# Performance work log

Measured on AMD Instinct MI355X. Metric: run time of the kernel, lower is better.

## Reference

```python
import jax, jax.numpy as jnp
import numpy as np
from jax import lax

W_BITS = (8, 8, 8)  # per init_kwargs
BN_EPS = 1e-5
DN = ('NCHW', 'OIHW', 'NCHW')


def fake_quant(w, bits):
    # Symmetric per-tensor uniform quantization (LUT multiply is mathematically
    # a multiply against these quantized weights). STE pass-through.
    qmax = 2.0 ** (bits - 1) - 1.0
    scale = jnp.max(jnp.abs(w)) / qmax
    wq = jnp.round(w / scale) * scale
    return w + lax.stop_gradient(wq - w)


def batchnorm(x, gamma, beta):
    # training-mode BN: batch statistics over N,H,W per channel
    m = jnp.mean(x, axis=(0, 2, 3), keepdims=True)
    v = jnp.var(x, axis=(0, 2, 3), keepdims=True)
    g = gamma.reshape(1, -1, 1, 1)
    b = beta.reshape(1, -1, 1, 1)
    return (x - m) * lax.rsqrt(v + BN_EPS) * g + b


def qconv(x, w, b, bits, stride=1, padding=0):
    wq = fake_quant(w, bits)
    y = lax.conv_general_dilated(x, wq, (stride, stride),
                                 [(padding, padding), (padding, padding)],
                                 dimension_numbers=DN)
    return y + b.reshape(1, -1, 1, 1)


def setup_inputs() -> dict:
    key = jax.random.key(0)
    ks = jax.random.split(key, 8)
    B, Cin, H, W = 64, 512, 28, 28
    width, Cout = 128, 512
    return {
        'x': jax.random.normal(ks[0], (B, Cin, H, W), jnp.float32),
        'w1': jax.random.normal(ks[1], (width, Cin, 1, 1), jnp.float32) * 0.05,
        'b1': jax.random.normal(ks[2], (width,), jnp.float32) * 0.05,
        'gamma1': jnp.ones((width,), jnp.float32),
        'beta1': jnp.zeros((width,), jnp.float32),
        'w2': jax.random.normal(ks[3], (width, width, 3, 3), jnp.float32) * 0.05,
        'b2': jax.random.normal(ks[4], (width,), jnp.float32) * 0.05,
        'gamma2': jnp.ones((width,), jnp.float32),
        'beta2': jnp.zeros((width,), jnp.float32),
        'w3': jax.random.normal(ks[5], (Cout, width, 1, 1), jnp.float32) * 0.05,
        'b3': jax.random.normal(ks[6], (Cout,), jnp.float32) * 0.05,
        'gamma3': jnp.ones((Cout,), jnp.float32),
        'beta3': jnp.zeros((Cout,), jnp.float32),
    }


def reference(x, w1, b1, gamma1, beta1, w2, b2, gamma2, beta2,
              w3, b3, gamma3, beta3):
    identity = x
    out = jax.nn.relu(batchnorm(qconv(x, w1, b1, W_BITS[0]), gamma1, beta1))
    out = jax.nn.relu(batchnorm(qconv(out, w2, b2, W_BITS[1], stride=1, padding=1), gamma2, beta2))
    out = batchnorm(qconv(out, w3, b3, W_BITS[2]), gamma3, beta3)
    return jax.nn.relu(out + identity)
```

## Files before the change

kernel.cpp:

```cpp
#include <hip/hip_runtime.h>
#include <hip/hip_bf16.h>
#include <math.h>

#define HW 784
#define IW 28
#define NB 64
#define BN_EPS 1e-5f

typedef __attribute__((ext_vector_type(8))) short bf16x8;
typedef __attribute__((ext_vector_type(4))) float f32x4;

static __device__ __forceinline__ ushort f2bf(float f) {
    __hip_bfloat16 h = __float2bfloat16(f);
    return *reinterpret_cast<ushort*>(&h);
}
static __device__ __forceinline__ float bf2f(ushort u) {
    return __uint_as_float(((unsigned)u) << 16);
}

static __device__ __forceinline__ uint4 bn_pack(uint4 v,
    const float* __restrict__ rs, const float* __restrict__ sh, int c0)
{
    float4 ra = *reinterpret_cast<const float4*>(rs + c0);
    float4 rb = *reinterpret_cast<const float4*>(rs + c0 + 4);
    float4 sa = *reinterpret_cast<const float4*>(sh + c0);
    float4 sb = *reinterpret_cast<const float4*>(sh + c0 + 4);
    ushort* u = (ushort*)&v;
    u[0] = f2bf(fmaxf(fmaf(bf2f(u[0]), ra.x, sa.x), 0.f));
    u[1] = f2bf(fmaxf(fmaf(bf2f(u[1]), ra.y, sa.y), 0.f));
    u[2] = f2bf(fmaxf(fmaf(bf2f(u[2]), ra.z, sa.z), 0.f));
    u[3] = f2bf(fmaxf(fmaf(bf2f(u[3]), ra.w, sa.w), 0.f));
    u[4] = f2bf(fmaxf(fmaf(bf2f(u[4]), rb.x, sb.x), 0.f));
    u[5] = f2bf(fmaxf(fmaf(bf2f(u[5]), rb.y, sb.y), 0.f));
    u[6] = f2bf(fmaxf(fmaf(bf2f(u[6]), rb.z, sb.z), 0.f));
    u[7] = f2bf(fmaxf(fmaf(bf2f(u[7]), rb.w, sb.w), 0.f));
    return v;
}

__global__ void absmax3_kernel(const float* __restrict__ w1,
                               const float* __restrict__ w2,
                               const float* __restrict__ w3,
                               unsigned int* __restrict__ slots) {
    const int t = blockIdx.y;
    const float* w = t == 0 ? w1 : (t == 1 ? w2 : w3);
    const int n = (t == 1) ? 147456 : 65536;
    float m = 0.f;
    for (int i = blockIdx.x * blockDim.x + threadIdx.x; i < n;
         i += gridDim.x * blockDim.x)
        m = fmaxf(m, fabsf(w[i]));
#pragma unroll
    for (int off = 32; off > 0; off >>= 1)
        m = fmaxf(m, __shfl_down(m, off, 64));
    __shared__ float sm[4];
    int lane = threadIdx.x & 63, wid = threadIdx.x >> 6;
    if (lane == 0) sm[wid] = m;
    __syncthreads();
    if (threadIdx.x == 0) {
        float b = fmaxf(fmaxf(sm[0], sm[1]), fmaxf(sm[2], sm[3]));
        atomicMax(slots + t, __float_as_uint(b));
    }
}

__global__ void prequant3_kernel(const float* __restrict__ w1,
                                 const float* __restrict__ w2,
                                 const float* __restrict__ w3,
                                 const unsigned int* __restrict__ amax,
                                 ushort* __restrict__ o1,
                                 ushort* __restrict__ o2,
                                 ushort* __restrict__ o3) {
    const int t = blockIdx.y;
    const float* w = t == 0 ? w1 : (t == 1 ? w2 : w3);
    ushort* o = t == 0 ? o1 : (t == 1 ? o2 : o3);
    const int n = (t == 1) ? 147456 : 65536;
    float am = __uint_as_float(amax[t]);
    float scale = am * (1.0f / 127.0f);
    float inv   = 127.0f / am;
    for (int i = blockIdx.x * blockDim.x + threadIdx.x; i < n;
         i += gridDim.x * blockDim.x) {
        float q = rintf(w[i] * inv) * scale;
        if (t == 1) {
            int co  = i / 1152;
            int rem = i - co * 1152;
            int ci  = rem / 9;
            int r   = rem - ci * 9;
            o[co * 1152 + r * 128 + ci] = f2bf(q);
        } else {
            o[i] = f2bf(q);
        }
    }
}

__device__ __forceinline__ void epi_t(
    f32x4 (*acc)[7], ushort* __restrict__ yt_img, float* __restrict__ part,
    int C, int pb, int co0, int colane, int lanehi)
{
#pragma unroll
    for (int fi = 0; fi < 2; ++fi) {
#pragma unroll
        for (int j = 0; j < 7; ++j) {
            int hw = j * 16 + colane;
            int co = co0 + fi * 16 + lanehi * 4;
            ushort4 u;
            u.x = f2bf(acc[fi][j][0]); u.y = f2bf(acc[fi][j][1]);
            u.z = f2bf(acc[fi][j][2]); u.w = f2bf(acc[fi][j][3]);
            *reinterpret_cast<ushort4*>(&yt_img[(size_t)hw * C + co]) = u;
        }
        float s[4] = {0, 0, 0, 0}, q[4] = {0, 0, 0, 0};
#pragma unroll
        for (int j = 0; j < 7; ++j)
#pragma unroll
            for (int r = 0; r < 4; ++r) {
                float v = acc[fi][j][r];
                s[r] += v; q[r] += v * v;
            }
#pragma unroll
        for (int m = 1; m < 16; m <<= 1)
#pragma unroll
            for (int r = 0; r < 4; ++r) {
                s[r] += __shfl_xor(s[r], m, 64);
                q[r] += __shfl_xor(q[r], m, 64);
            }
        if (colane == 0) {
#pragma unroll
            for (int r = 0; r < 4; ++r) {
                int co = co0 + fi * 16 + lanehi * 4 + r;
                part[(size_t)co * 448 + pb]       = s[r];
                part[(size_t)(C + co) * 448 + pb] = q[r];
            }
        }
    }
}

__global__ __launch_bounds__(256, 2) void conv1_mfma(
    const float* __restrict__ X, const ushort* __restrict__ Wq,
    ushort* __restrict__ y1t, float* __restrict__ part)
{
    __shared__ ushort lds[2][112 * 40];
    const int n = blockIdx.z, hwt = blockIdx.x;
    const int tid = threadIdx.x, lane = tid & 63, wv = tid >> 6;
    const int colane = lane & 15, lanehi = lane >> 4, klane = lanehi * 8;
    const float* __restrict__ Xn = X + (size_t)n * 512 * HW + hwt * 112;

    int s_hw[4], s_cg[4];
#pragma unroll
    for (int it = 0; it < 4; ++it) {
        int idx = tid + it * 256;
        s_hw[it] = idx % 112; s_cg[it] = idx / 112;
    }
    float4 rv[4];

    auto sload = [&](int kt) {
#pragma unroll
        for (int it = 0; it < 4; ++it) {
            if (it == 3 && tid >= 128) continue;
            const float* xp = Xn + (size_t)(kt * 32 + s_cg[it] * 4) * HW + s_hw[it];
            rv[it].x = xp[0];
            rv[it].y = xp[HW];
            rv[it].z = xp[2 * HW];
            rv[it].w = xp[3 * HW];
        }
    };
    auto swrite = [&](int b) {
#pragma unroll
        for (int it = 0; it < 4; ++it) {
            if (it == 3 && tid >= 128) continue;
            ushort4 u;
            u.x = f2bf(rv[it].x); u.y = f2bf(rv[it].y);
            u.z = f2bf(rv[it].z); u.w = f2bf(rv[it].w);
            *reinterpret_cast<ushort4*>(&lds[b][s_hw[it] * 40 + s_cg[it] * 4]) = u;
        }
    };

    f32x4 acc[2][7];
#pragma unroll
    for (int i = 0; i < 2; ++i)
#pragma unroll
        for (int j = 0; j < 7; ++j) acc[i][j] = (f32x4)(0.f);

    const ushort* A0 = Wq + (size_t)(wv * 32 + colane) * 512 + klane;

    sload(0); swrite(0); __syncthreads();
    for (int kt = 0; kt < 16; ++kt) {
        if (kt < 15) sload(kt + 1);
        const int b = kt & 1;
        bf16x8 a0 = *reinterpret_cast<const bf16x8*>(A0 + kt * 32);
        bf16x8 a1 = *reinterpret_cast<const bf16x8*>(A0 + 16 * 512 + kt * 32);
#pragma unroll
        for (int j = 0; j < 7; ++j) {
            bf16x8 bb = *reinterpret_cast<const bf16x8*>(
                &lds[b][(j * 16 + colane) * 40 + klane]);
            acc[0][j] = __builtin_amdgcn_mfma_f32_16x16x32_bf16(a0, bb, acc[0][j], 0, 0, 0);
            acc[1][j] = __builtin_amdgcn_mfma_f32_16x16x32_bf16(a1, bb, acc[1][j], 0, 0, 0);
        }
        if (kt < 15) swrite(b ^ 1);
        __syncthreads();
    }
    epi_t(acc, y1t + (size_t)n * HW * 128 + (size_t)hwt * 112 * 128, part,
          128, n * 7 + hwt, wv * 32, colane, lanehi);
}

__global__ __launch_bounds__(256, 2) void conv2_mfma(
    const ushort* __restrict__ y1t, const ushort* __restrict__ Wq,
    ushort* __restrict__ y2t, float* __restrict__ part,
    const float* __restrict__ rs1, const float* __restrict__ sh1)
{
    __shared__ ushort lds[2][2 * 6 * 30 * 40];
    const int n = blockIdx.z, hwt = blockIdx.x;
    const int tid = threadIdx.x, lane = tid & 63, wv = tid >> 6;
    const int colane = lane & 15, lanehi = lane >> 4, klane = lanehi * 8;
    const size_t noff = (size_t)n * HW * 128;
    const int h0 = hwt * 4;

    auto stage = [&](int p, int b) {
        for (int s = tid; s < 1440; s += 256) {
            int rr = s / 240, rem = s - rr * 240, ww = rem >> 3, sl = rem & 7;
            int cc = sl >> 2, g = sl & 3;
            int h = h0 - 1 + rr, w = ww - 1;
            int c0 = (2 * p + cc) * 32 + g * 8;
            uint4 v = make_uint4(0, 0, 0, 0);
            if ((unsigned)h < IW && (unsigned)w < IW) {
                v = *reinterpret_cast<const uint4*>(
                    &y1t[noff + (size_t)(h * IW + w) * 128 + c0]);
                v = bn_pack(v, rs1, sh1, c0);
            }
            *reinterpret_cast<uint4*>(&lds[b][((cc * 6 + rr) * 30 + ww) * 40 + g * 8]) = v;
        }
    };

    int base[7];
#pragma unroll
    for (int j = 0; j < 7; ++j) {
        int hwl = j * 16 + colane;
        int hl = hwl / 28, wl = hwl - hl * 28;
        base[j] = ((hl + 1) * 30 + (wl + 1)) * 40 + klane;
    }

    f32x4 acc[2][7];
#pragma unroll
    for (int i = 0; i < 2; ++i)
#pragma unroll
        for (int j = 0; j < 7; ++j) acc[i][j] = (f32x4)(0.f);

    const ushort* A0 = Wq + (size_t)(wv * 32 + colane) * 1152 + klane;

    auto compute = [&](int p, int b) {
        for (int r = 0; r < 9; ++r) {
            const int dh = r / 3 - 1, dw = r - (r / 3) * 3 - 1;
            const int delta = (dh * 30 + dw) * 40;
#pragma unroll
            for (int cc = 0; cc < 2; ++cc) {
                bf16x8 a0 = *reinterpret_cast<const bf16x8*>(
                    A0 + r * 128 + (2 * p + cc) * 32);
                bf16x8 a1 = *reinterpret_cast<const bf16x8*>(
                    A0 + 16 * 1152 + r * 128 + (2 * p + cc) * 32);
                const ushort* L = &lds[b][cc * 7200];
#pragma unroll
                for (int j = 0; j < 7; ++j) {
                    bf16x8 bb = *reinterpret_cast<const bf16x8*>(&L[base[j] + delta]);
                    acc[0][j] = __builtin_amdgcn_mfma_f32_16x16x32_bf16(a0, bb, acc[0][j], 0, 0, 0);
                    acc[1][j] = __builtin_amdgcn_mfma_f32_16x16x32_bf16(a1, bb, acc[1][j], 0, 0, 0);
                }
            }
        }
    };

    stage(0, 0);
    __syncthreads();

    uint4 pv[6];
#pragma unroll
    for (int it = 0; it < 6; ++it) {
        int s = tid + it * 256;
        if (it == 5 && tid >= 160) continue;
        int rr = s / 240, rem = s - rr * 240, ww = rem >> 3, sl = rem & 7;
        int cc = sl >> 2, g = sl & 3;
        int h = h0 - 1 + rr, w = ww - 1;
        int c0 = (2 + cc) * 32 + g * 8;
        uint4 v = make_uint4(0, 0, 0, 0);
        if ((unsigned)h < IW && (unsigned)w < IW) {
            v = *reinterpret_cast<const uint4*>(
                &y1t[noff + (size_t)(h * IW + w) * 128 + c0]);
            v = bn_pack(v, rs1, sh1, c0);
        }
        pv[it] = v;
    }

    compute(0, 0);

#pragma unroll
    for (int it = 0; it < 6; ++it) {
        int s = tid + it * 256;
        if (it == 5 && tid >= 160) continue;
        int rr = s / 240, rem = s - rr * 240, ww = rem >> 3, sl = rem & 7;
        int cc = sl >> 2, g = sl & 3;
        *reinterpret_cast<uint4*>(&lds[1][((cc * 6 + rr) * 30 + ww) * 40 + g * 8]) = pv[it];
    }
    __syncthreads();
    compute(1, 1);

    epi_t(acc, y2t + noff + (size_t)hwt * 112 * 128, part,
          128, n * 7 + hwt, wv * 32, colane, lanehi);
}

template <int BF16OUT>
__global__ __launch_bounds__(256, 2) void conv3_mfma(
    const ushort* __restrict__ y2t, const ushort* __restrict__ Wq,
    void* __restrict__ yout, float* __restrict__ part,
    const float* __restrict__ rs2, const float* __restrict__ sh2)
{
    __shared__ ushort B_lds[112 * 136];
    const int n = blockIdx.z, hwt = blockIdx.x;
    const int tid = threadIdx.x, lane = tid & 63, wv = tid >> 6;
    const int colane = lane & 15, lanehi = lane >> 4, klane = lanehi * 8;
    const size_t noff = (size_t)n * HW * 128;

    for (int s = tid; s < 1792; s += 256) {
        int hw = s >> 4, g = s & 15, c0 = g * 8;
        uint4 v = *reinterpret_cast<const uint4*>(
            &y2t[noff + (size_t)(hwt * 112 + hw) * 128 + c0]);
        v = bn_pack(v, rs2, sh2, c0);
        *reinterpret_cast<uint4*>(&B_lds[hw * 136 + c0]) = v;
    }
    __syncthreads();

#pragma unroll 1
    for (int cot = 0; cot < 4; ++cot) {
        const int co0 = cot * 128 + wv * 32;
        f32x4 acc[2][7];
#pragma unroll
        for (int i = 0; i < 2; ++i)
#pragma unroll
            for (int j = 0; j < 7; ++j) acc[i][j] = (f32x4)(0.f);

        const ushort* A0 = Wq + (size_t)(co0 + colane) * 128 + klane;
#pragma unroll
        for (int kt = 0; kt < 4; ++kt) {
            bf16x8 a0 = *reinterpret_cast<const bf16x8*>(A0 + kt * 32);
            bf16x8 a1 = *reinterpret_cast<const bf16x8*>(A0 + 16 * 128 + kt * 32);
#pragma unroll
            for (int j = 0; j < 7; ++j) {
                bf16x8 bb = *reinterpret_cast<const bf16x8*>(
                    &B_lds[(j * 16 + colane) * 136 + kt * 32 + klane]);
                acc[0][j] = __builtin_amdgcn_mfma_f32_16x16x32_bf16(a0, bb, acc[0][j], 0, 0, 0);
                acc[1][j] = __builtin_amdgcn_mfma_f32_16x16x32_bf16(a1, bb, acc[1][j], 0, 0, 0);
            }
        }

#pragma unroll
        for (int fi = 0; fi < 2; ++fi) {
#pragma unroll
            for (int j = 0; j < 7; ++j) {
                int cob = co0 + fi * 16 + lanehi * 4;
                int hw = hwt * 112 + j * 16 + colane;
#pragma unroll
                for (int r = 0; r < 4; ++r) {
                    float v = acc[fi][j][r];
                    if (BF16OUT)
                        ((ushort*)yout)[((size_t)n * 512 + cob + r) * HW + hw] = f2bf(v);
                    else
                        ((float*)yout)[((size_t)n * 512 + cob + r) * HW + hw] = v;
                }
            }
            float s[4] = {0, 0, 0, 0}, q[4] = {0, 0, 0, 0};
#pragma unroll
            for (int j = 0; j < 7; ++j)
#pragma unroll
                for (int r = 0; r < 4; ++r) {
                    float v = acc[fi][j][r];
                    s[r] += v; q[r] += v * v;
                }
#pragma unroll
            for (int m = 1; m < 16; m <<= 1)
#pragma unroll
                for (int r = 0; r < 4; ++r) {
                    s[r] += __shfl_xor(s[r], m, 64);
                    q[r] += __shfl_xor(q[r], m, 64);
                }
            if (colane == 0) {
#pragma unroll
                for (int r = 0; r < 4; ++r) {
                    int co = co0 + fi * 16 + lanehi * 4 + r;
                    part[(size_t)co * 448 + (n * 7 + hwt)]         = s[r];
                    part[(size_t)(512 + co) * 448 + (n * 7 + hwt)] = q[r];
                }
            }
        }
    }
}

__global__ void finalize_stats(const float* __restrict__ part, int C,
    const float* __restrict__ gamma, const float* __restrict__ beta,
    float* __restrict__ rs, float* __restrict__ sh)
{
    int c = blockIdx.x, lane = threadIdx.x;
    double s = 0.0, s2 = 0.0;
    for (int i = lane; i < 448; i += 64) {
        s  += part[(size_t)c * 448 + i];
        s2 += part[(size_t)(C + c) * 448 + i];
    }
#pragma unroll
    for (int m = 1; m < 64; m <<= 1) {
        s  += __shfl_xor(s, m, 64);
        s2 += __shfl_xor(s2, m, 64);
    }
    if (lane == 0) {
        double tot = (double)NB * HW;
        double mean = s / tot;
        float var = (float)(s2 / tot - mean * mean);
        float r = rsqrtf(var + BN_EPS) * gamma[c];
        rs[c] = r;
        sh[c] = beta[c] - (float)mean * r;
    }
}

__global__ void final_f32(float* __restrict__ out, const float* __restrict__ x,
    const float* __restrict__ rs, const float* __restrict__ sh)
{
    int i = blockIdx.x * blockDim.x + threadIdx.x;
    if (i >= NB * 512 * (HW / 4)) return;
    int c = (i / (HW / 4)) & 511;
    float r = rs[c], s = sh[c];
    float4 v = reinterpret_cast<float4*>(out)[i];
    float4 xv = reinterpret_cast<const float4*>(x)[i];
    v.x = fmaxf(fmaf(v.x, r, s) + xv.x, 0.f);
    v.y = fmaxf(fmaf(v.y, r, s) + xv.y, 0.f);
    v.z = fmaxf(fmaf(v.z, r, s) + xv.z, 0.f);
    v.w = fmaxf(fmaf(v.w, r, s) + xv.w, 0.f);
    reinterpret_cast<float4*>(out)[i] = v;
}

__global__ void final_b16(float* __restrict__ out, const float* __restrict__ x,
    const ushort* __restrict__ y3,
    const float* __restrict__ rs, const float* __restrict__ sh)
{
    int i = blockIdx.x * blockDim.x + threadIdx.x;
    if (i >= NB * 512 * 98) return;
    int c = (i / 98) & 511;
    float r = rs[c], s = sh[c];
    uint4 yv = reinterpret_cast<const uint4*>(y3)[i];
    const ushort* u = (const ushort*)&yv;
    float4 x0 = reinterpret_cast<const float4*>(x)[2 * i];
    float4 x1 = reinterpret_cast<const float4*>(x)[2 * i + 1];
    float4 o0, o1;
    o0.x = fmaxf(fmaf(bf2f(u[0]), r, s) + x0.x, 0.f);
    o0.y = fmaxf(fmaf(bf2f(u[1]), r, s) + x0.y, 0.f);
    o0.z = fmaxf(fmaf(bf2f(u[2]), r, s) + x0.z, 0.f);
    o0.w = fmaxf(fmaf(bf2f(u[3]), r, s) + x0.w, 0.f);
    o1.x = fmaxf(fmaf(bf2f(u[4]), r, s) + x1.x, 0.f);
    o1.y = fmaxf(fmaf(bf2f(u[5]), r, s) + x1.y, 0.f);
    o1.z = fmaxf(fmaf(bf2f(u[6]), r, s) + x1.z, 0.f);
    o1.w = fmaxf(fmaf(bf2f(u[7]), r, s) + x1.w, 0.f);
    reinterpret_cast<float4*>(out)[2 * i] = o0;
    reinterpret_cast<float4*>(out)[2 * i + 1] = o1;
}

extern "C" void kernel_launch(void* const* d_in, const int* in_sizes, int n_in,
                              void* d_out, int out_size, void* d_ws, size_t ws_size,
                              hipStream_t stream)
{
    const float* x   = (const float*)d_in[0];
    const float* w1  = (const float*)d_in[1];
    const float* g1  = (const float*)d_in[3];
    const float* be1 = (const float*)d_in[4];
    const float* w2  = (const float*)d_in[5];
    const float* g2  = (const float*)d_in[7];
    const float* be2 = (const float*)d_in[8];
    const float* w3  = (const float*)d_in[9];
    const float* g3  = (const float*)d_in[11];
    const float* be3 = (const float*)d_in[12];
    float* out = (float*)d_out;

    char* wsb = (char*)d_ws;
    unsigned int* amax = (unsigned int*)wsb;
    float* rs1 = (float*)(wsb + 1024);
    float* sh1 = (float*)(wsb + 1536);
    float* rs2 = (float*)(wsb + 2048);
    float* sh2 = (float*)(wsb + 2560);
    float* rs3 = (float*)(wsb + 3072);
    float* sh3 = (float*)(wsb + 5120);
    float* part1 = (float*)(wsb + 8192);
    float* part2 = (float*)(wsb + 466944);
    float* part3 = (float*)(wsb + 925696);
    ushort* Wq1 = (ushort*)(wsb + 2760704);
    ushort* Wq2 = (ushort*)(wsb + 2891776);
    ushort* Wq3 = (ushort*)(wsb + 3186688);
    ushort* y1t = (ushort*)(wsb + 3317760);
    ushort* y2t = (ushort*)(wsb + 16162816);
    ushort* y3b = (ushort*)(wsb + 29007872);

    const bool big = ws_size >= (size_t)82000000;

    hipMemsetAsync(amax, 0, 64, stream);
    absmax3_kernel<<<dim3(32, 3), 256, 0, stream>>>(w1, w2, w3, amax);
    prequant3_kernel<<<dim3(96, 3), 256, 0, stream>>>(w1, w2, w3, amax,
                                                      Wq1, Wq2, Wq3);

    conv1_mfma<<<dim3(7, 1, NB), 256, 0, stream>>>(x, Wq1, y1t, part1);
    finalize_stats<<<128, 64, 0, stream>>>(part1, 128, g1, be1, rs1, sh1);

    conv2_mfma<<<dim3(7, 1, NB), 256, 0, stream>>>(y1t, Wq2, y2t, part2,
                                                   rs1, sh1);
    finalize_stats<<<128, 64, 0, stream>>>(part2, 128, g2, be2, rs2, sh2);

    if (big) {
        conv3_mfma<1><<<dim3(7, 1, NB), 256, 0, stream>>>(y2t, Wq3, y3b,
                                                          part3, rs2, sh2);
        finalize_stats<<<512, 64, 0, stream>>>(part3, 512, g3, be3, rs3, sh3);
        final_b16<<<12544, 256, 0, stream>>>(out, x, y3b, rs3, sh3);
    } else {
        conv3_mfma<0><<<dim3(7, 1, NB), 256, 0, stream>>>(y2t, Wq3, out,
                                                          part3, rs2, sh2);
        finalize_stats<<<512, 64, 0, stream>>>(part3, 512, g3, be3, rs3, sh3);
        final_f32<<<25088, 256, 0, stream>>>(out, x, rs3, sh3);
    }
}
```

Measured before the change: 153.0 us.

## Recompute conv3 instead of materializing its output; fuse BN3+residual+ReLU epilogue

```diff
diff --git a/kernel.cpp b/kernel.cpp
--- a/kernel.cpp
+++ b/kernel.cpp
@@ -293,7 +293,8 @@
         if (it == 5 && tid >= 160) continue;
         int rr = s / 240, rem = s - rr * 240, ww = rem >> 3, sl = rem & 7;
         int cc = sl >> 2, g = sl & 3;
-        *reinterpret_cast<uint4*>(&lds[1][((cc * 6 + rr) * 30 + ww) * 40 + g * 8]) = pv[it];
+        *reinterpret_cast<uint4*>(
+            &lds[1][((cc * 6 + rr) * 30 + ww) * 40 + g * 8]) = pv[it];
     }
     __syncthreads();
     compute(1, 1);
@@ -302,10 +303,9 @@
           128, n * 7 + hwt, wv * 32, colane, lanehi);
 }
 
-template <int BF16OUT>
-__global__ __launch_bounds__(256, 2) void conv3_mfma(
+__global__ __launch_bounds__(256, 2) void conv3_stats(
     const ushort* __restrict__ y2t, const ushort* __restrict__ Wq,
-    void* __restrict__ yout, float* __restrict__ part,
+    float* __restrict__ part,
     const float* __restrict__ rs2, const float* __restrict__ sh2)
 {
     __shared__ ushort B_lds[112 * 136];
@@ -348,19 +348,6 @@
 
 #pragma unroll
         for (int fi = 0; fi < 2; ++fi) {
-#pragma unroll
-            for (int j = 0; j < 7; ++j) {
-                int cob = co0 + fi * 16 + lanehi * 4;
-                int hw = hwt * 112 + j * 16 + colane;
-#pragma unroll
-                for (int r = 0; r < 4; ++r) {
-                    float v = acc[fi][j][r];
-                    if (BF16OUT)
-                        ((ushort*)yout)[((size_t)n * 512 + cob + r) * HW + hw] = f2bf(v);
-                    else
-                        ((float*)yout)[((size_t)n * 512 + cob + r) * HW + hw] = v;
-                }
-            }
             float s[4] = {0, 0, 0, 0}, q[4] = {0, 0, 0, 0};
 #pragma unroll
             for (int j = 0; j < 7; ++j)
@@ -385,6 +372,88 @@
                 }
             }
         }
+    }
+}
+
+__global__ __launch_bounds__(256, 2) void conv3_final(
+    const ushort* __restrict__ y2t, const ushort* __restrict__ Wq,
+    const float* __restrict__ X, float* __restrict__ out,
+    const float* __restrict__ rs2, const float* __restrict__ sh2,
+    const float* __restrict__ rs3, const float* __restrict__ sh3)
+{
+    __shared__ ushort B_lds[112 * 136];
+    __shared__ ushort O_lds[128 * 120];
+    __shared__ float  C_lds[1024];
+    const int n = blockIdx.z, hwt = blockIdx.x;
+    const int tid = threadIdx.x, lane = tid & 63, wv = tid >> 6;
+    const int colane = lane & 15, lanehi = lane >> 4, klane = lanehi * 8;
+    const size_t noff = (size_t)n * HW * 128;
+
+    for (int s = tid; s < 1792; s += 256) {
+        int hw = s >> 4, g = s & 15, c0 = g * 8;
+        uint4 v = *reinterpret_cast<const uint4*>(
+            &y2t[noff + (size_t)(hwt * 112 + hw) * 128 + c0]);
+        v = bn_pack(v, rs2, sh2, c0);
+        *reinterpret_cast<uint4*>(&B_lds[hw * 136 + c0]) = v;
+    }
+    for (int i = tid; i < 1024; i += 256)
+        C_lds[i] = (i < 512) ? rs3[i] : sh3[i - 512];
+    __syncthreads();
+
+#pragma unroll 1
+    for (int cot = 0; cot < 4; ++cot) {
+        const int co0 = cot * 128 + wv * 32;
+        f32x4 acc[2][7];
+#pragma unroll
+        for (int i = 0; i < 2; ++i)
+#pragma unroll
+            for (int j = 0; j < 7; ++j) acc[i][j] = (f32x4)(0.f);
+
+        const ushort* A0 = Wq + (size_t)(co0 + colane) * 128 + klane;
+#pragma unroll
+        for (int kt = 0; kt < 4; ++kt) {
+            bf16x8 a0 = *reinterpret_cast<const bf16x8*>(A0 + kt * 32);
+            bf16x8 a1 = *reinterpret_cast<const bf16x8*>(A0 + 16 * 128 + kt * 32);
+#pragma unroll
+            for (int j = 0; j < 7; ++j) {
+                bf16x8 bb = *reinterpret_cast<const bf16x8*>(
+                    &B_lds[(j * 16 + colane) * 136 + kt * 32 + klane]);
+                acc[0][j] = __builtin_amdgcn_mfma_f32_16x16x32_bf16(a0, bb, acc[0][j], 0, 0, 0);
+                acc[1][j] = __builtin_amdgcn_mfma_f32_16x16x32_bf16(a1, bb, acc[1][j], 0, 0, 0);
+            }
+        }
+
+#pragma unroll
+        for (int fi = 0; fi < 2; ++fi)
+#pragma unroll
+            for (int j = 0; j < 7; ++j) {
+                int rowb = (wv * 32 + fi * 16 + lanehi * 4) * 120 + j * 16 + colane;
+#pragma unroll
+                for (int r = 0; r < 4; ++r)
+                    O_lds[rowb + r * 120] = f2bf(acc[fi][j][r]);
+            }
+        __syncthreads();
+
+        const float* xb = X + ((size_t)n * 512 + cot * 128) * HW + hwt * 112;
+        float* ob = out + ((size_t)n * 512 + cot * 128) * HW + hwt * 112;
+#pragma unroll
+        for (int it = 0; it < 14; ++it) {
+            int slot = it * 256 + tid;
+            int row = slot / 28, c4 = slot - row * 28;
+            float r3 = C_lds[cot * 128 + row];
+            float s3 = C_lds[512 + cot * 128 + row];
+            ushort4 yv = *reinterpret_cast<const ushort4*>(
+                &O_lds[row * 120 + c4 * 4]);
+            float4 xv = *reinterpret_cast<const float4*>(
+                xb + (size_t)row * HW + c4 * 4);
+            float4 o;
+            o.x = fmaxf(fmaf(bf2f(yv.x), r3, s3) + xv.x, 0.f);
+            o.y = fmaxf(fmaf(bf2f(yv.y), r3, s3) + xv.y, 0.f);
+            o.z = fmaxf(fmaf(bf2f(yv.z), r3, s3) + xv.z, 0.f);
+            o.w = fmaxf(fmaf(bf2f(yv.w), r3, s3) + xv.w, 0.f);
+            *reinterpret_cast<float4*>(ob + (size_t)row * HW + c4 * 4) = o;
+        }
+        __syncthreads();
     }
 }
 
@@ -411,47 +480,6 @@
         rs[c] = r;
         sh[c] = beta[c] - (float)mean * r;
     }
-}
-
-__global__ void final_f32(float* __restrict__ out, const float* __restrict__ x,
-    const float* __restrict__ rs, const float* __restrict__ sh)
-{
-    int i = blockIdx.x * blockDim.x + threadIdx.x;
-    if (i >= NB * 512 * (HW / 4)) return;
-    int c = (i / (HW / 4)) & 511;
-    float r = rs[c], s = sh[c];
-    float4 v = reinterpret_cast<float4*>(out)[i];
-    float4 xv = reinterpret_cast<const float4*>(x)[i];
-    v.x = fmaxf(fmaf(v.x, r, s) + xv.x, 0.f);
-    v.y = fmaxf(fmaf(v.y, r, s) + xv.y, 0.f);
-    v.z = fmaxf(fmaf(v.z, r, s) + xv.z, 0.f);
-    v.w = fmaxf(fmaf(v.w, r, s) + xv.w, 0.f);
-    reinterpret_cast<float4*>(out)[i] = v;
-}
-
-__global__ void final_b16(float* __restrict__ out, const float* __restrict__ x,
-    const ushort* __restrict__ y3,
-    const float* __restrict__ rs, const float* __restrict__ sh)
-{
-    int i = blockIdx.x * blockDim.x + threadIdx.x;
-    if (i >= NB * 512 * 98) return;
-    int c = (i / 98) & 511;
-    float r = rs[c], s = sh[c];
-    uint4 yv = reinterpret_cast<const uint4*>(y3)[i];
-    const ushort* u = (const ushort*)&yv;
-    float4 x0 = reinterpret_cast<const float4*>(x)[2 * i];
-    float4 x1 = reinterpret_cast<const float4*>(x)[2 * i + 1];
-    float4 o0, o1;
-    o0.x = fmaxf(fmaf(bf2f(u[0]), r, s) + x0.x, 0.f);
-    o0.y = fmaxf(fmaf(bf2f(u[1]), r, s) + x0.y, 0.f);
-    o0.z = fmaxf(fmaf(bf2f(u[2]), r, s) + x0.z, 0.f);
-    o0.w = fmaxf(fmaf(bf2f(u[3]), r, s) + x0.w, 0.f);
-    o1.x = fmaxf(fmaf(bf2f(u[4]), r, s) + x1.x, 0.f);
-    o1.y = fmaxf(fmaf(bf2f(u[5]), r, s) + x1.y, 0.f);
-    o1.z = fmaxf(fmaf(bf2f(u[6]), r, s) + x1.z, 0.f);
-    o1.w = fmaxf(fmaf(bf2f(u[7]), r, s) + x1.w, 0.f);
-    reinterpret_cast<float4*>(out)[2 * i] = o0;
-    reinterpret_cast<float4*>(out)[2 * i + 1] = o1;
 }
 
 extern "C" void kernel_launch(void* const* d_in, const int* in_sizes, int n_in,
@@ -486,11 +514,8 @@
     ushort* Wq3 = (ushort*)(wsb + 3186688);
     ushort* y1t = (ushort*)(wsb + 3317760);
     ushort* y2t = (ushort*)(wsb + 16162816);
-    ushort* y3b = (ushort*)(wsb + 29007872);
-
-    const bool big = ws_size >= (size_t)82000000;
-
-    hipMemsetAsync(amax, 0, 64, stream);
+
+    (void)hipMemsetAsync(amax, 0, 64, stream);
     absmax3_kernel<<<dim3(32, 3), 256, 0, stream>>>(w1, w2, w3, amax);
     prequant3_kernel<<<dim3(96, 3), 256, 0, stream>>>(w1, w2, w3, amax,
                                                       Wq1, Wq2, Wq3);
@@ -502,15 +527,9 @@
                                                    rs1, sh1);
     finalize_stats<<<128, 64, 0, stream>>>(part2, 128, g2, be2, rs2, sh2);
 
-    if (big) {
-        conv3_mfma<1><<<dim3(7, 1, NB), 256, 0, stream>>>(y2t, Wq3, y3b,
-                                                          part3, rs2, sh2);
-        finalize_stats<<<512, 64, 0, stream>>>(part3, 512, g3, be3, rs3, sh3);
-        final_b16<<<12544, 256, 0, stream>>>(out, x, y3b, rs3, sh3);
-    } else {
-        conv3_mfma<0><<<dim3(7, 1, NB), 256, 0, stream>>>(y2t, Wq3, out,
-                                                          part3, rs2, sh2);
-        finalize_stats<<<512, 64, 0, stream>>>(part3, 512, g3, be3, rs3, sh3);
-        final_f32<<<25088, 256, 0, stream>>>(out, x, rs3, sh3);
-    }
-}
+    conv3_stats<<<dim3(7, 1, NB), 256, 0, stream>>>(y2t, Wq3, part3, rs2, sh2);
+    finalize_stats<<<512, 64, 0, stream>>>(part3, 512, g3, be3, rs3, sh3);
+
+    conv3_final<<<dim3(7, 1, NB), 256, 0, stream>>>(y2t, Wq3, x, out,
+                                                    rs2, sh2, rs3, sh3);
+}
```

Result: faster. 142.2 us (-7.0%).
